# Performance work log

Measured on AMD Instinct MI355X. Metric: run time of the kernel, lower is better.

Reference implementation:

```python
import jax, jax.numpy as jnp
import numpy as np

OUT_FEATURES = 4096
IN_FEATURES = 4096
R = 16
DIST = 4
N_FREQ = 10000
SCALING = 150.0


def setup_inputs() -> dict:
    key = jax.random.key(0)
    k_x, k_w, k_b, k_s, k_a, k_i = jax.random.split(key, 6)
    x = jax.random.normal(k_x, (4, 2048, IN_FEATURES), dtype=jnp.float32)
    base_w = jax.random.normal(k_w, (OUT_FEATURES, IN_FEATURES), dtype=jnp.float32) * 0.02
    base_b = jax.random.normal(k_b, (OUT_FEATURES,), dtype=jnp.float32) * 0.02
    spectrum = jax.random.normal(k_s, (N_FREQ,), dtype=jnp.float32)
    hora_A = jax.random.normal(k_a, (R, IN_FEATURES), dtype=jnp.float32)
    # torch uses randperm(r*out_features)[:n_frequency] -> unique flat indices
    idx = jax.random.permutation(k_i, R * OUT_FEATURES)[:N_FREQ].astype(jnp.int32)
    return {"x": x, "base_w": base_w, "base_b": base_b,
            "spectrum": spectrum, "hora_A": hora_A, "idx": idx}


def reference(x, base_w, base_b, spectrum, hora_A, idx):
    # --- get_delta_weight ---
    rows = idx // R            # index into out_features
    cols = idx % R             # index into r
    dense_spectrum = jnp.zeros((OUT_FEATURES, R), dtype=spectrum.dtype)
    dense_spectrum = dense_spectrum.at[rows, cols].set(spectrum)
    # chunk_size = ceil(out/dist) = 1024; out divisible by dist -> pure reshape
    chunks = dense_spectrum.reshape(DIST, OUT_FEATURES // DIST, R)
    B = jnp.fft.ifft2(chunks, axes=(-2, -1)).real.astype(spectrum.dtype)
    B = B.reshape(OUT_FEATURES, R)
    delta_w = (B * SCALING) @ hora_A          # [out_features, in_features]
    # --- forward: base linear + adapter linear ---
    base_out = jnp.einsum('bsi,oi->bso', x, base_w) + base_b
    result = base_out + jnp.einsum('bsi,oi->bso', x, delta_w)
    return result
```

## Files before the change

kernel.cpp:

```cpp
#include <hip/hip_runtime.h>
#include <hip/hip_bf16.h>


#define OUTF 4096
#define INF  4096
#define NFREQ 10000
#define MDIM 8192
#define KT   (INF / 64)

typedef __attribute__((ext_vector_type(8)))  short bf16x8;
typedef __attribute__((ext_vector_type(16))) float f32x16;

__device__ __forceinline__ unsigned int bf16pack2(float a, float b) {
    unsigned int ua = __builtin_bit_cast(unsigned int, a);
    unsigned int ub = __builtin_bit_cast(unsigned int, b);
    ua = (ua + 0x7fffu + ((ua >> 16) & 1u)) >> 16;
    ub = (ub + 0x7fffu + ((ub >> 16) & 1u)) & 0xffff0000u;
    return ua | ub;
}

__device__ __forceinline__ void async_copy16(const void* g, void* l) {
    __builtin_amdgcn_global_load_lds(
        (__attribute__((address_space(1))) void*)(g),
        (__attribute__((address_space(3))) void*)(l),
        16, 0, 0);
}

__global__ __launch_bounds__(256) void compact_kernel(
        const float* __restrict__ spectrum, const int* __restrict__ idx,
        int2* __restrict__ cjk, int* __restrict__ ccnt) {
    const int p   = blockIdx.x;
    const int tid = threadIdx.x;
    const int wv  = tid >> 6, ln = tid & 63;
    __shared__ int wcnt[4];
    int cnt = 0;
    for (int i0 = wv * 64; i0 < NFREQ; i0 += 256) {
        const int i = i0 + ln;
        bool m = (i < NFREQ) && ((idx[i] >> 14) == p);
        cnt += __popcll(__ballot(m));
    }
    if (ln == 0) wcnt[wv] = cnt;
    __syncthreads();
    int base = 0;
    for (int w = 0; w < wv; ++w) base += wcnt[w];
    for (int i0 = wv * 64; i0 < NFREQ; i0 += 256) {
        const int i = i0 + ln;
        bool m = false; int id = 0;
        if (i < NFREQ) { id = idx[i]; m = ((id >> 14) == p); }
        unsigned long long bal = __ballot(m);
        if (m) {
            int pos = base + __popcll(bal & ((1ull << ln) - 1ull));
            if (pos < 4096)
                cjk[p * 4096 + pos] =
                    make_int2(id & 16383, __builtin_bit_cast(int, spectrum[i]));
        }
        base += __popcll(bal);
    }
    if (tid == 0) {
        int t = wcnt[0] + wcnt[1] + wcnt[2] + wcnt[3];
        ccnt[p] = (t < 4096) ? t : 4096;
    }
}

__global__ __launch_bounds__(256) void buildB_kernel(
        const int2* __restrict__ cjk, const int* __restrict__ ccnt,
        float* __restrict__ Bout) {
    __shared__ int2  s_jkv[4096];
    __shared__ float s_part[4][64];
    const int tid  = threadIdx.x;
    const int gid0 = blockIdx.x * 64;
    const int p    = gid0 >> 14;
    const int cnt  = ccnt[p];
    for (int t = tid; t < cnt; t += 256) s_jkv[t] = cjk[p * 4096 + t];
    __syncthreads();
    const int qtr  = tid >> 6;
    const int ol   = tid & 63;
    const int gid  = gid0 + ol;
    const int o    = gid >> 4;
    const int r    = gid & 15;
    const int m    = o & 1023;
    const int qlen = (cnt + 3) >> 2;
    const int t0   = qtr * qlen;
    const int t1   = (t0 + qlen < cnt) ? t0 + qlen : cnt;
    const float c  = 6.283185307179586f / 16384.f;
    float acc = 0.f;
    for (int t = t0; t < t1; ++t) {
        const int2 jv = s_jkv[t];
        const int j = jv.x >> 4, k = jv.x & 15;
        int ph = (((j * m) & 1023) << 4) + (((k * r) & 15) << 10);
        acc += __builtin_bit_cast(float, jv.y) * __cosf((float)(ph & 16383) * c);
    }
    s_part[qtr][ol] = acc;
    __syncthreads();
    if (tid < 64) {
        float s = s_part[0][tid] + s_part[1][tid] + s_part[2][tid] + s_part[3][tid];
        Bout[gid0 + tid] = s * (150.f / 16384.f);
    }
}

__global__ __launch_bounds__(256) void build_w_kernel(
        const float* __restrict__ bw, const float* __restrict__ A,
        const float* __restrict__ Bs, unsigned short* __restrict__ W) {
    const int n0 = blockIdx.x * 8;
    __shared__ float sB[8][16];
    if (threadIdx.x < 128)
        ((float*)sB)[threadIdx.x] = Bs[n0 * 16 + threadIdx.x];
    __syncthreads();
    const float4* A4 = (const float4*)A;
    const float4* bw4 = (const float4*)bw;
    uint2* W2 = (uint2*)W;
#pragma unroll 1
    for (int q = 0; q < 4; ++q) {
        const int c4 = threadIdx.x + q * 256;
        float4 a[16];
#pragma unroll
        for (int r = 0; r < 16; ++r) a[r] = A4[r * 1024 + c4];
#pragma unroll 1
        for (int nn = 0; nn < 8; ++nn) {
            const int n = n0 + nn;
            float4 wv = bw4[n * 1024 + c4];
#pragma unroll
            for (int r = 0; r < 16; ++r) {
                float s = sB[nn][r];
                wv.x += s * a[r].x; wv.y += s * a[r].y;
                wv.z += s * a[r].z; wv.w += s * a[r].w;
            }
            W2[n * 1024 + c4] = make_uint2(bf16pack2(wv.x, wv.y),
                                           bf16pack2(wv.z, wv.w));
        }
    }
}

__global__ __launch_bounds__(256) void cvt_x_kernel(
        const float4* __restrict__ x, uint2* __restrict__ xb, int n4) {
    for (int i = blockIdx.x * blockDim.x + threadIdx.x; i < n4;
         i += gridDim.x * blockDim.x) {
        float4 v = x[i];
        xb[i] = make_uint2(bf16pack2(v.x, v.y), bf16pack2(v.z, v.w));
    }
}

__global__ __launch_bounds__(512, 2) void gemm256_kernel(
        const unsigned short* __restrict__ Xb,
        const unsigned short* __restrict__ Wb,
        const float* __restrict__ bias, float* __restrict__ C) {
    __shared__ __align__(1024) char lds[131072];

    const int tid  = threadIdx.x;
    const int lane = tid & 63;
    const int wid  = tid >> 6;
    const int wm   = wid >> 2;
    const int wn   = wid & 3;

    int bid = blockIdx.x;
    bid = (bid & 7) * 64 + (bid >> 3);
    const int tm = bid >> 4;
    const int tn = bid & 15;
    const int arow0 = tm * 256;
    const int brow0 = tn * 256;

    const int srow  = tid >> 3;
    const int scole = (((tid & 7) * 16) ^ ((srow & 7) << 4)) >> 1;
    const int sldsb = tid * 16;

    const int l31 = lane & 31;
    const int kxr = ((lane >> 5) << 4) ^ ((lane & 7) << 4);
    const int abase = (wm * 128 + l31) * 128;
    const int bbase = 32768 + (wn * 64 + l31) * 128;

    f32x16 acc[4][2] = {};
    bf16x8 af[4][2], bf[2][2];

#define STAGE_HALF(mat, grow0, t, ldsbase) do {                               \
        const unsigned short* _s =                                            \
            (mat) + ((grow0) + srow) * INF + (t) * 64 + scole;                \
        async_copy16(_s, lds + (ldsbase) + sldsb);                            \
        async_copy16(_s + 64 * INF, lds + (ldsbase) + 8192 + sldsb);          \
    } while (0)

#define LDA(DB, f, ks) (*(const bf16x8*)(lds + (DB) + abase + (f) * 4096 + (((ks) << 5) ^ kxr)))
#define LDB(DB, n, ks) (*(const bf16x8*)(lds + (DB) + bbase + (n) * 4096 + (((ks) << 5) ^ kxr)))
#define MFMA(a, b, c) __builtin_amdgcn_mfma_f32_32x32x16_bf16((a), (b), (c), 0, 0, 0)
#define BARRIER() do { asm volatile("" ::: "memory");                         \
                       __builtin_amdgcn_s_barrier();                          \
                       asm volatile("" ::: "memory"); } while (0)

#define TILE(CUR, OTH, s) do {                                                \
                   \
    _Pragma("unroll") for (int f = 0; f < 4; ++f) {                           \
        af[f][0] = LDA(CUR, f, 0); af[f][1] = LDA(CUR, f, 1); }               \
    _Pragma("unroll") for (int n = 0; n < 2; ++n) {                           \
        bf[n][0] = LDB(CUR, n, 0); bf[n][1] = LDB(CUR, n, 1); }               \
    if ((s) + 1 < KT) {                                                       \
        STAGE_HALF(Xb, arow0,       (s) + 1, (OTH) + 0);                      \
        STAGE_HALF(Xb, arow0 + 128, (s) + 1, (OTH) + 16384);                  \
    }                                                                         \
    asm volatile("s_waitcnt lgkmcnt(0)" ::: "memory");                        \
    BARRIER();                                                                \
    __builtin_amdgcn_s_setprio(1);                                            \
    _Pragma("unroll") for (int ks = 0; ks < 2; ++ks)                          \
        _Pragma("unroll") for (int f = 0; f < 4; ++f)                         \
            _Pragma("unroll") for (int n = 0; n < 2; ++n)                     \
                acc[f][n] = MFMA(af[f][ks], bf[n][ks], acc[f][n]);            \
    __builtin_amdgcn_s_setprio(0);                                            \
    BARRIER();                                                                \
              \
    _Pragma("unroll") for (int f = 0; f < 4; ++f) {                           \
        af[f][0] = LDA(CUR, f, 2); af[f][1] = LDA(CUR, f, 3); }               \
    _Pragma("unroll") for (int n = 0; n < 2; ++n) {                           \
        bf[n][0] = LDB(CUR, n, 2); bf[n][1] = LDB(CUR, n, 3); }               \
    asm volatile("s_waitcnt lgkmcnt(0)" ::: "memory");                        \
    BARRIER();                                                                \
    if ((s) + 2 < KT) {                                                       \
        STAGE_HALF(Wb, brow0,       (s) + 2, (CUR) + 32768);                  \
        STAGE_HALF(Wb, brow0 + 128, (s) + 2, (CUR) + 49152);                  \
    }                                                                         \
    __builtin_amdgcn_s_setprio(1);                                            \
    _Pragma("unroll") for (int ks = 0; ks < 2; ++ks)                          \
        _Pragma("unroll") for (int f = 0; f < 4; ++f)                         \
            _Pragma("unroll") for (int n = 0; n < 2; ++n)                     \
                acc[f][n] = MFMA(af[f][ks], bf[n][ks], acc[f][n]);            \
    __builtin_amdgcn_s_setprio(0);                                            \
    if ((s) + 2 < KT) { asm volatile("s_waitcnt vmcnt(4)" ::: "memory"); }    \
    else              { asm volatile("s_waitcnt vmcnt(0)" ::: "memory"); }    \
    BARRIER();                                                                \
} while (0)

    STAGE_HALF(Xb, arow0,       0, 0);
    STAGE_HALF(Xb, arow0 + 128, 0, 16384);
    STAGE_HALF(Wb, brow0,       0, 32768);
    STAGE_HALF(Wb, brow0 + 128, 0, 49152);
    STAGE_HALF(Wb, brow0,       1, 65536 + 32768);
    STAGE_HALF(Wb, brow0 + 128, 1, 65536 + 49152);
    asm volatile("s_waitcnt vmcnt(4)" ::: "memory");
    BARRIER();

    for (int s = 0; s < KT; s += 2) {
        TILE(0, 65536, s);
        TILE(65536, 0, s + 1);
    }

#pragma unroll
    for (int n = 0; n < 2; ++n) {
        const int gcol = brow0 + wn * 64 + n * 32 + l31;
        const float bv = bias[gcol];
#pragma unroll
        for (int f = 0; f < 4; ++f) {
            const int rbase = arow0 + wm * 128 + f * 32 + 4 * (lane >> 5);
#pragma unroll
            for (int reg = 0; reg < 16; ++reg) {
                const int grow = rbase + (reg & 3) + 8 * (reg >> 2);
                C[grow * OUTF + gcol] = acc[f][n][reg] + bv;
            }
        }
    }
#undef STAGE_HALF
#undef LDA
#undef LDB
#undef MFMA
#undef BARRIER
#undef TILE
}

extern "C" void kernel_launch(void* const* d_in, const int* in_sizes, int n_in,
                              void* d_out, int out_size, void* d_ws, size_t ws_size,
                              hipStream_t stream) {
    const float* x    = (const float*)d_in[0];
    const float* bw   = (const float*)d_in[1];
    const float* bb   = (const float*)d_in[2];
    const float* spec = (const float*)d_in[3];
    const float* ha   = (const float*)d_in[4];
    const int*   idx  = (const int*)d_in[5];
    float* out = (float*)d_out;

    char* ws = (char*)d_ws;
    float*          Bbuf = (float*)ws;
    unsigned short* Wb   = (unsigned short*)(ws + 262144);
    unsigned short* Xb   = (unsigned short*)(ws + 262144 + 33554432);
    int2*           cjk  = (int2*)(ws + 262144 + 33554432 + 67108864);
    int*            ccnt = (int*)(ws + 262144 + 33554432 + 67108864 + 131072);

    compact_kernel<<<4, 256, 0, stream>>>(spec, idx, cjk, ccnt);
    buildB_kernel<<<1024, 256, 0, stream>>>(cjk, ccnt, Bbuf);
    build_w_kernel<<<512, 256, 0, stream>>>(bw, ha, Bbuf, Wb);
    cvt_x_kernel<<<2048, 256, 0, stream>>>((const float4*)x, (uint2*)Xb,
                                           (MDIM * INF) / 4);
    gemm256_kernel<<<512, 512, 0, stream>>>(Xb, Wb, bb, out);
}
```

Before: 466.2 us.

## Switch GEMM to 16x16x32 MFMA and restructure per-tile LDS pipeline

Replaces the 32x32x16 bf16 MFMA with 16x16x32 MFMA, which changes the per-wave fragment layout to 8x4 accumulator tiles and the LDS read addressing. The tile loop is also reworked so each K-step loads all A and B fragments up front and prefetches both X and W for the next stage together. This drops the two-phase schedule with staggered W prefetch and the extra barriers. The cost is a full vmcnt(0) wait per tile, which weakens overlap between global loads and compute, and more fragment registers.

```diff
diff --git a/kernel.cpp b/kernel.cpp
--- a/kernel.cpp
+++ b/kernel.cpp
@@ -8,8 +8,8 @@
 #define MDIM 8192
 #define KT   (INF / 64)
 
-typedef __attribute__((ext_vector_type(8)))  short bf16x8;
-typedef __attribute__((ext_vector_type(16))) float f32x16;
+typedef __attribute__((ext_vector_type(8))) short bf16x8;
+typedef __attribute__((ext_vector_type(4))) float f32x4;
 
 __device__ __forceinline__ unsigned int bf16pack2(float a, float b) {
     unsigned int ua = __builtin_bit_cast(unsigned int, a);
@@ -163,13 +163,14 @@
     const int scole = (((tid & 7) * 16) ^ ((srow & 7) << 4)) >> 1;
     const int sldsb = tid * 16;
 
-    const int l31 = lane & 31;
-    const int kxr = ((lane >> 5) << 4) ^ ((lane & 7) << 4);
-    const int abase = (wm * 128 + l31) * 128;
-    const int bbase = 32768 + (wn * 64 + l31) * 128;
-
-    f32x16 acc[4][2] = {};
-    bf16x8 af[4][2], bf[2][2];
+    const int l15 = lane & 15;
+    const int kx0 = ((lane >> 4) * 16) ^ ((lane & 7) << 4);
+    const int kx1 = kx0 ^ 64;
+    const int abase0 = (wm * 128 + l15) * 128;
+    const int bbase0 = 32768 + (wn * 64 + l15) * 128;
+
+    f32x4 acc[8][4] = {};
+    bf16x8 af[8][2], bf[4][2];
 
 #define STAGE_HALF(mat, grow0, t, ldsbase) do {                               \
         const unsigned short* _s =                                            \
@@ -178,51 +179,40 @@
         async_copy16(_s + 64 * INF, lds + (ldsbase) + 8192 + sldsb);          \
     } while (0)
 
-#define LDA(DB, f, ks) (*(const bf16x8*)(lds + (DB) + abase + (f) * 4096 + (((ks) << 5) ^ kxr)))
-#define LDB(DB, n, ks) (*(const bf16x8*)(lds + (DB) + bbase + (n) * 4096 + (((ks) << 5) ^ kxr)))
-#define MFMA(a, b, c) __builtin_amdgcn_mfma_f32_32x32x16_bf16((a), (b), (c), 0, 0, 0)
+#define LDA(DB, m, kh) (*(const bf16x8*)(lds + (DB) + abase0 + (m) * 2048 + ((kh) ? kx1 : kx0)))
+#define LDB(DB, n, kh) (*(const bf16x8*)(lds + (DB) + bbase0 + (n) * 2048 + ((kh) ? kx1 : kx0)))
+#define MFMA(a, b, c) __builtin_amdgcn_mfma_f32_16x16x32_bf16((a), (b), (c), 0, 0, 0)
 #define BARRIER() do { asm volatile("" ::: "memory");                         \
                        __builtin_amdgcn_s_barrier();                          \
                        asm volatile("" ::: "memory"); } while (0)
 
 #define TILE(CUR, OTH, s) do {                                                \
-                   \
-    _Pragma("unroll") for (int f = 0; f < 4; ++f) {                           \
-        af[f][0] = LDA(CUR, f, 0); af[f][1] = LDA(CUR, f, 1); }               \
-    _Pragma("unroll") for (int n = 0; n < 2; ++n) {                           \
-        bf[n][0] = LDB(CUR, n, 0); bf[n][1] = LDB(CUR, n, 1); }               \
+                           \
+    _Pragma("unroll") for (int m = 0; m < 4; ++m) af[m][0] = LDA(CUR, m, 0);  \
+    _Pragma("unroll") for (int n = 0; n < 4; ++n) bf[n][0] = LDB(CUR, n, 0);  \
+    _Pragma("unroll") for (int m = 4; m < 8; ++m) af[m][0] = LDA(CUR, m, 0);  \
+    _Pragma("unroll") for (int n = 0; n < 4; ++n) bf[n][1] = LDB(CUR, n, 1);  \
+    _Pragma("unroll") for (int m = 0; m < 8; ++m) af[m][1] = LDA(CUR, m, 1);  \
+                                         \
     if ((s) + 1 < KT) {                                                       \
         STAGE_HALF(Xb, arow0,       (s) + 1, (OTH) + 0);                      \
         STAGE_HALF(Xb, arow0 + 128, (s) + 1, (OTH) + 16384);                  \
+        STAGE_HALF(Wb, brow0,       (s) + 1, (OTH) + 32768);                  \
+        STAGE_HALF(Wb, brow0 + 128, (s) + 1, (OTH) + 49152);                  \
     }                                                                         \
-    asm volatile("s_waitcnt lgkmcnt(0)" ::: "memory");                        \
-    BARRIER();                                                                \
+           \
     __builtin_amdgcn_s_setprio(1);                                            \
-    _Pragma("unroll") for (int ks = 0; ks < 2; ++ks)                          \
-        _Pragma("unroll") for (int f = 0; f < 4; ++f)                         \
-            _Pragma("unroll") for (int n = 0; n < 2; ++n)                     \
-                acc[f][n] = MFMA(af[f][ks], bf[n][ks], acc[f][n]);            \
+    _Pragma("unroll") for (int m = 0; m < 4; ++m)                             \
+        _Pragma("unroll") for (int n = 0; n < 4; ++n)                         \
+            acc[m][n] = MFMA(af[m][0], bf[n][0], acc[m][n]);                  \
+    _Pragma("unroll") for (int m = 4; m < 8; ++m)                             \
+        _Pragma("unroll") for (int n = 0; n < 4; ++n)                         \
+            acc[m][n] = MFMA(af[m][0], bf[n][0], acc[m][n]);                  \
+    _Pragma("unroll") for (int m = 0; m < 8; ++m)                             \
+        _Pragma("unroll") for (int n = 0; n < 4; ++n)                         \
+            acc[m][n] = MFMA(af[m][1], bf[n][1], acc[m][n]);                  \
     __builtin_amdgcn_s_setprio(0);                                            \
-    BARRIER();                                                                \
-              \
-    _Pragma("unroll") for (int f = 0; f < 4; ++f) {                           \
-        af[f][0] = LDA(CUR, f, 2); af[f][1] = LDA(CUR, f, 3); }               \
-    _Pragma("unroll") for (int n = 0; n < 2; ++n) {                           \
-        bf[n][0] = LDB(CUR, n, 2); bf[n][1] = LDB(CUR, n, 3); }               \
-    asm volatile("s_waitcnt lgkmcnt(0)" ::: "memory");                        \
-    BARRIER();                                                                \
-    if ((s) + 2 < KT) {                                                       \
-        STAGE_HALF(Wb, brow0,       (s) + 2, (CUR) + 32768);                  \
-        STAGE_HALF(Wb, brow0 + 128, (s) + 2, (CUR) + 49152);                  \
-    }                                                                         \
-    __builtin_amdgcn_s_setprio(1);                                            \
-    _Pragma("unroll") for (int ks = 0; ks < 2; ++ks)                          \
-        _Pragma("unroll") for (int f = 0; f < 4; ++f)                         \
-            _Pragma("unroll") for (int n = 0; n < 2; ++n)                     \
-                acc[f][n] = MFMA(af[f][ks], bf[n][ks], acc[f][n]);            \
-    __builtin_amdgcn_s_setprio(0);                                            \
-    if ((s) + 2 < KT) { asm volatile("s_waitcnt vmcnt(4)" ::: "memory"); }    \
-    else              { asm volatile("s_waitcnt vmcnt(0)" ::: "memory"); }    \
+    asm volatile("s_waitcnt vmcnt(0)" ::: "memory");                          \
     BARRIER();                                                                \
 } while (0)
 
@@ -230,9 +220,7 @@
     STAGE_HALF(Xb, arow0 + 128, 0, 16384);
     STAGE_HALF(Wb, brow0,       0, 32768);
     STAGE_HALF(Wb, brow0 + 128, 0, 49152);
-    STAGE_HALF(Wb, brow0,       1, 65536 + 32768);
-    STAGE_HALF(Wb, brow0 + 128, 1, 65536 + 49152);
-    asm volatile("s_waitcnt vmcnt(4)" ::: "memory");
+    asm volatile("s_waitcnt vmcnt(0)" ::: "memory");
     BARRIER();
 
     for (int s = 0; s < KT; s += 2) {
@@ -241,17 +229,15 @@
     }
 
 #pragma unroll
-    for (int n = 0; n < 2; ++n) {
-        const int gcol = brow0 + wn * 64 + n * 32 + l31;
+    for (int n = 0; n < 4; ++n) {
+        const int gcol = brow0 + wn * 64 + n * 16 + l15;
         const float bv = bias[gcol];
 #pragma unroll
-        for (int f = 0; f < 4; ++f) {
-            const int rbase = arow0 + wm * 128 + f * 32 + 4 * (lane >> 5);
-#pragma unroll
-            for (int reg = 0; reg < 16; ++reg) {
-                const int grow = rbase + (reg & 3) + 8 * (reg >> 2);
-                C[grow * OUTF + gcol] = acc[f][n][reg] + bv;
-            }
+        for (int m = 0; m < 8; ++m) {
+            const int grow = arow0 + wm * 128 + m * 16 + (lane >> 4) * 4;
+#pragma unroll
+            for (int rg = 0; rg < 4; ++rg)
+                C[(grow + rg) * OUTF + gcol] = acc[m][n][rg] + bv;
         }
     }
 #undef STAGE_HALF
```

New measurement: 530.6 us. 13.8% more time.

## Fuse x conversion into B build and reschedule GEMM into quarter-phase pipeline

Applied to the files above, without the earlier changes.

The x-to-bf16 conversion is folded into the spectrum/B construction kernel, which removes one launch and lets the conversion overlap the cosine-sum work. The GEMM main loop is restructured into four phases per K tile. Each phase loads part of the A and B fragments and issues one quarter of the MFMAs, with global-to-LDS staging spread across the phases and a vmcnt(2) wait instead of vmcnt(4). The LDS swizzle pattern is also changed to use a different row-bit XOR. The extra barriers and the changed wait and swizzle logic add synchronisation overhead and some risk of bank conflicts or ordering mistakes.

```diff
diff --git a/kernel.cpp b/kernel.cpp
--- a/kernel.cpp
+++ b/kernel.cpp
@@ -62,9 +62,10 @@
     }
 }
 
-__global__ __launch_bounds__(256) void buildB_kernel(
+__global__ __launch_bounds__(256) void buildB_cvt_kernel(
         const int2* __restrict__ cjk, const int* __restrict__ ccnt,
-        float* __restrict__ Bout) {
+        float* __restrict__ Bout,
+        const float4* __restrict__ x4, uint2* __restrict__ xb) {
     __shared__ int2  s_jkv[4096];
     __shared__ float s_part[4][64];
     const int tid  = threadIdx.x;
@@ -96,6 +97,11 @@
         float s = s_part[0][tid] + s_part[1][tid] + s_part[2][tid] + s_part[3][tid];
         Bout[gid0 + tid] = s * (150.f / 16384.f);
     }
+    const int n4 = (MDIM * INF) / 4;
+    for (int i = blockIdx.x * 256 + tid; i < n4; i += 1024 * 256) {
+        float4 v = x4[i];
+        xb[i] = make_uint2(bf16pack2(v.x, v.y), bf16pack2(v.z, v.w));
+    }
 }
 
 __global__ __launch_bounds__(256) void build_w_kernel(
@@ -131,15 +137,6 @@
     }
 }
 
-__global__ __launch_bounds__(256) void cvt_x_kernel(
-        const float4* __restrict__ x, uint2* __restrict__ xb, int n4) {
-    for (int i = blockIdx.x * blockDim.x + threadIdx.x; i < n4;
-         i += gridDim.x * blockDim.x) {
-        float4 v = x[i];
-        xb[i] = make_uint2(bf16pack2(v.x, v.y), bf16pack2(v.z, v.w));
-    }
-}
-
 __global__ __launch_bounds__(512, 2) void gemm256_kernel(
         const unsigned short* __restrict__ Xb,
         const unsigned short* __restrict__ Wb,
@@ -159,17 +156,20 @@
     const int arow0 = tm * 256;
     const int brow0 = tn * 256;
 
+    const int scole = (((tid & 7) << 4) ^ (((tid >> 5) & 7) << 4)) >> 1;
     const int srow  = tid >> 3;
-    const int scole = (((tid & 7) * 16) ^ ((srow & 7) << 4)) >> 1;
     const int sldsb = tid * 16;
 
     const int l31 = lane & 31;
-    const int kxr = ((lane >> 5) << 4) ^ ((lane & 7) << 4);
+    const int kxr = ((lane >> 5) << 4) ^ (((l31 >> 2) & 7) << 4);
     const int abase = (wm * 128 + l31) * 128;
     const int bbase = 32768 + (wn * 64 + l31) * 128;
 
     f32x16 acc[4][2] = {};
-    bf16x8 af[4][2], bf[2][2];
+    bf16x8 af[2][4], bfa[4], bfb[4];
+
+#define BUF_E 0
+#define BUF_O 65536
 
 #define STAGE_HALF(mat, grow0, t, ldsbase) do {                               \
         const unsigned short* _s =                                            \
@@ -184,61 +184,79 @@
 #define BARRIER() do { asm volatile("" ::: "memory");                         \
                        __builtin_amdgcn_s_barrier();                          \
                        asm volatile("" ::: "memory"); } while (0)
-
-#define TILE(CUR, OTH, s) do {                                                \
-                   \
-    _Pragma("unroll") for (int f = 0; f < 4; ++f) {                           \
-        af[f][0] = LDA(CUR, f, 0); af[f][1] = LDA(CUR, f, 1); }               \
-    _Pragma("unroll") for (int n = 0; n < 2; ++n) {                           \
-        bf[n][0] = LDB(CUR, n, 0); bf[n][1] = LDB(CUR, n, 1); }               \
-    if ((s) + 1 < KT) {                                                       \
-        STAGE_HALF(Xb, arow0,       (s) + 1, (OTH) + 0);                      \
-        STAGE_HALF(Xb, arow0 + 128, (s) + 1, (OTH) + 16384);                  \
-    }                                                                         \
-    asm volatile("s_waitcnt lgkmcnt(0)" ::: "memory");                        \
+#define PH_SYNC() do { BARRIER();                                             \
+                       asm volatile("s_waitcnt lgkmcnt(0)" ::: "memory");     \
+                       __builtin_amdgcn_sched_barrier(0); } while (0)
+
+#define RD_BFA(DB)  _Pragma("unroll") for (int ks = 0; ks < 4; ++ks)          \
+                        bfa[ks] = LDB(DB, 0, ks);
+#define RD_BFB(DB)  _Pragma("unroll") for (int ks = 0; ks < 4; ++ks)          \
+                        bfb[ks] = LDB(DB, 1, ks);
+#define RD_AF01(DB) _Pragma("unroll") for (int j = 0; j < 2; ++j)             \
+                        _Pragma("unroll") for (int ks = 0; ks < 4; ++ks)      \
+                            af[j][ks] = LDA(DB, j, ks);
+#define RD_AF23(DB) _Pragma("unroll") for (int j = 0; j < 2; ++j)             \
+                        _Pragma("unroll") for (int ks = 0; ks < 4; ++ks)      \
+                            af[j][ks] = LDA(DB, j + 2, ks);
+
+#define QMFMA(fh, n, B)                                                       \
+    __builtin_amdgcn_s_setprio(1);                                            \
+    _Pragma("unroll") for (int ks = 0; ks < 4; ++ks)                          \
+        _Pragma("unroll") for (int j = 0; j < 2; ++j)                         \
+            acc[(fh) * 2 + j][n] =                                            \
+                MFMA(af[j][ks], (B)[ks], acc[(fh) * 2 + j][n]);               \
+    __builtin_amdgcn_s_setprio(0)
+
+#define PAIR(s) do {                                                          \
+                                               \
+    RD_BFA(BUF_E); RD_AF01(BUF_E);                                            \
+    STAGE_HALF(Xb, arow0,       (s) + 1, BUF_O + 0);                          \
+    PH_SYNC(); QMFMA(0, 0, bfa); BARRIER();                                   \
+                                               \
+    RD_BFB(BUF_E);                                                            \
+    STAGE_HALF(Xb, arow0 + 128, (s) + 1, BUF_O + 16384);                      \
+    PH_SYNC(); QMFMA(0, 1, bfb); BARRIER();                                   \
+                                             \
+    RD_AF23(BUF_E);                                                           \
+    if ((s) + 2 < KT) STAGE_HALF(Wb, brow0, (s) + 2, BUF_E + 32768);          \
+    PH_SYNC(); QMFMA(1, 0, bfa); BARRIER();                                   \
+                                   \
+    if ((s) + 2 < KT) STAGE_HALF(Wb, brow0 + 128, (s) + 2, BUF_E + 49152);    \
+    PH_SYNC(); QMFMA(1, 1, bfb);                                              \
+    if ((s) + 2 < KT) { asm volatile("s_waitcnt vmcnt(2)" ::: "memory"); }    \
+    else              { asm volatile("s_waitcnt vmcnt(0)" ::: "memory"); }    \
     BARRIER();                                                                \
-    __builtin_amdgcn_s_setprio(1);                                            \
-    _Pragma("unroll") for (int ks = 0; ks < 2; ++ks)                          \
-        _Pragma("unroll") for (int f = 0; f < 4; ++f)                         \
-            _Pragma("unroll") for (int n = 0; n < 2; ++n)                     \
-                acc[f][n] = MFMA(af[f][ks], bf[n][ks], acc[f][n]);            \
-    __builtin_amdgcn_s_setprio(0);                                            \
-    BARRIER();                                                                \
-              \
-    _Pragma("unroll") for (int f = 0; f < 4; ++f) {                           \
-        af[f][0] = LDA(CUR, f, 2); af[f][1] = LDA(CUR, f, 3); }               \
-    _Pragma("unroll") for (int n = 0; n < 2; ++n) {                           \
-        bf[n][0] = LDB(CUR, n, 2); bf[n][1] = LDB(CUR, n, 3); }               \
-    asm volatile("s_waitcnt lgkmcnt(0)" ::: "memory");                        \
-    BARRIER();                                                                \
-    if ((s) + 2 < KT) {                                                       \
-        STAGE_HALF(Wb, brow0,       (s) + 2, (CUR) + 32768);                  \
-        STAGE_HALF(Wb, brow0 + 128, (s) + 2, (CUR) + 49152);                  \
-    }                                                                         \
-    __builtin_amdgcn_s_setprio(1);                                            \
-    _Pragma("unroll") for (int ks = 0; ks < 2; ++ks)                          \
-        _Pragma("unroll") for (int f = 0; f < 4; ++f)                         \
-            _Pragma("unroll") for (int n = 0; n < 2; ++n)                     \
-                acc[f][n] = MFMA(af[f][ks], bf[n][ks], acc[f][n]);            \
-    __builtin_amdgcn_s_setprio(0);                                            \
-    if ((s) + 2 < KT) { asm volatile("s_waitcnt vmcnt(4)" ::: "memory"); }    \
+                                             \
+    RD_BFA(BUF_O); RD_AF01(BUF_O);                                            \
+    if ((s) + 2 < KT) STAGE_HALF(Xb, arow0, (s) + 2, BUF_E + 0);              \
+    PH_SYNC(); QMFMA(0, 0, bfa); BARRIER();                                   \
+                                             \
+    RD_BFB(BUF_O);                                                            \
+    if ((s) + 2 < KT) STAGE_HALF(Xb, arow0 + 128, (s) + 2, BUF_E + 16384);    \
+    PH_SYNC(); QMFMA(0, 1, bfb); BARRIER();                                   \
+                                             \
+    RD_AF23(BUF_O);                                                           \
+    if ((s) + 3 < KT) STAGE_HALF(Wb, brow0, (s) + 3, BUF_O + 32768);          \
+    PH_SYNC(); QMFMA(1, 0, bfa); BARRIER();                                   \
+                                   \
+    if ((s) + 3 < KT) STAGE_HALF(Wb, brow0 + 128, (s) + 3, BUF_O + 49152);    \
+    PH_SYNC(); QMFMA(1, 1, bfb);                                              \
+    if ((s) + 3 < KT) { asm volatile("s_waitcnt vmcnt(2)" ::: "memory"); }    \
     else              { asm volatile("s_waitcnt vmcnt(0)" ::: "memory"); }    \
     BARRIER();                                                                \
 } while (0)
 
-    STAGE_HALF(Xb, arow0,       0, 0);
-    STAGE_HALF(Xb, arow0 + 128, 0, 16384);
-    STAGE_HALF(Wb, brow0,       0, 32768);
-    STAGE_HALF(Wb, brow0 + 128, 0, 49152);
-    STAGE_HALF(Wb, brow0,       1, 65536 + 32768);
-    STAGE_HALF(Wb, brow0 + 128, 1, 65536 + 49152);
-    asm volatile("s_waitcnt vmcnt(4)" ::: "memory");
+    STAGE_HALF(Wb, brow0,       0, BUF_E + 32768);
+    STAGE_HALF(Wb, brow0 + 128, 0, BUF_E + 49152);
+    STAGE_HALF(Xb, arow0,       0, BUF_E + 0);
+    STAGE_HALF(Xb, arow0 + 128, 0, BUF_E + 16384);
+    STAGE_HALF(Wb, brow0,       1, BUF_O + 32768);
+    STAGE_HALF(Wb, brow0 + 128, 1, BUF_O + 49152);
+    asm volatile("s_waitcnt vmcnt(0)" ::: "memory");
     BARRIER();
 
-    for (int s = 0; s < KT; s += 2) {
-        TILE(0, 65536, s);
-        TILE(65536, 0, s + 1);
-    }
+    for (int s = 0; s < KT; s += 2)
+        PAIR(s);
 
 #pragma unroll
     for (int n = 0; n < 2; ++n) {
@@ -259,7 +277,15 @@
 #undef LDB
 #undef MFMA
 #undef BARRIER
-#undef TILE
+#undef PH_SYNC
+#undef RD_BFA
+#undef RD_BFB
+#undef RD_AF01
+#undef RD_AF23
+#undef QMFMA
+#undef PAIR
+#undef BUF_E
+#undef BUF_O
 }
 
 extern "C" void kernel_launch(void* const* d_in, const int* in_sizes, int n_in,
@@ -281,9 +307,8 @@
     int*            ccnt = (int*)(ws + 262144 + 33554432 + 67108864 + 131072);
 
     compact_kernel<<<4, 256, 0, stream>>>(spec, idx, cjk, ccnt);
-    buildB_kernel<<<1024, 256, 0, stream>>>(cjk, ccnt, Bbuf);
+    buildB_cvt_kernel<<<1024, 256, 0, stream>>>(cjk, ccnt, Bbuf,
+                                                (const float4*)x, (uint2*)Xb);
     build_w_kernel<<<512, 256, 0, stream>>>(bw, ha, Bbuf, Wb);
-    cvt_x_kernel<<<2048, 256, 0, stream>>>((const float4*)x, (uint2*)Xb,
-                                           (MDIM * INF) / 4);
     gemm256_kernel<<<512, 512, 0, stream>>>(Xb, Wb, bb, out);
 }
```

Result: faster. 415.9 us (-10.8%).
